# Optimization experiments

Hardware: AMD Instinct MI355X
Metric: run time of the kernel (lower is better)

The kernel has to match this reference:

```python
import jax, jax.numpy as jnp
import numpy as np

N_NODES = 50000
N_EDGES = 800000
IN_C = 64
HID = 128
OUT_C = 2
N_GRAPHS = 64


def setup_inputs() -> dict:
    key = jax.random.key(0)
    ks = jax.random.split(key, 12)
    x = jax.random.normal(ks[0], (N_NODES, IN_C), dtype=jnp.float32)
    edge_index = jax.random.randint(ks[1], (2, N_EDGES), 0, N_NODES, dtype=jnp.int64)
    batch = jnp.sort(jax.random.randint(ks[2], (N_NODES,), 0, N_GRAPHS, dtype=jnp.int64))
    def glorot(k, shape):
        lim = float(np.sqrt(6.0 / (shape[0] + shape[1])))
        return jax.random.uniform(k, shape, dtype=jnp.float32, minval=-lim, maxval=lim)
    return {
        "x": x,
        "edge_index": edge_index,
        "batch": batch,
        "W1": glorot(ks[3], (IN_C, HID)),  "b1": jnp.zeros((HID,), jnp.float32),
        "W2": glorot(ks[4], (HID, HID)),   "b2": jnp.zeros((HID,), jnp.float32),
        "Wm1": glorot(ks[5], (HID, HID)),  "bm1": jnp.zeros((HID,), jnp.float32),
        "Wm2": glorot(ks[6], (HID, OUT_C)), "bm2": jnp.zeros((OUT_C,), jnp.float32),
    }


def reference(x, edge_index, batch, W1, b1, W2, b2, Wm1, bm1, Wm2, bm2):
    N = x.shape[0]
    # GCN normalization with self-loops (PyG GCNConv defaults)
    loops = jnp.arange(N, dtype=edge_index.dtype)
    src = jnp.concatenate([edge_index[0], loops])  # message sources
    dst = jnp.concatenate([edge_index[1], loops])  # aggregation targets
    deg = jax.ops.segment_sum(jnp.ones(dst.shape, x.dtype), dst, num_segments=N)
    dinv = jnp.where(deg > 0, jax.lax.rsqrt(deg), 0.0)
    norm = dinv[src] * dinv[dst]  # [E+N]

    def gcn_conv(h, W, b):
        h = h @ W                         # transform first (PyG order)
        msg = h[src] * norm[:, None]      # gather + normalize
        return jax.ops.segment_sum(msg, dst, num_segments=N) + b  # scatter-add

    h = jax.nn.relu(gcn_conv(x, W1, b1))
    # dropout is identity in eval mode
    h = gcn_conv(h, W2, b2)

    # global mean pool over graphs
    sums = jax.ops.segment_sum(h, batch, num_segments=N_GRAPHS)
    cnt = jax.ops.segment_sum(jnp.ones((N,), h.dtype), batch, num_segments=N_GRAPHS)
    g = sums / jnp.maximum(cnt, 1.0)[:, None]  # [G, HID]

    g = jax.nn.relu(g @ Wm1 + bm1)
    return g @ Wm2 + bm2  # [G, OUT_C]
```

## Files before the change

### kernel.cpp

```cpp
#include <hip/hip_runtime.h>
#include <stdint.h>

#define N_NODES 50000
#define N_EDGES 800000
#define IN_C 64
#define HID 128
#define OUT_C 2
#define N_GRAPHS 64
#define NBUCK 196
#define BCAP 6144
#define ECH 4096

typedef long long i64;
typedef __attribute__((ext_vector_type(8))) short bf8;
typedef __attribute__((ext_vector_type(4))) float f32x4;

__device__ __forceinline__ float bf2f(ushort h) {
    return __uint_as_float(((uint)h) << 16);
}
__device__ __forceinline__ ushort f2bf(float f) {
    uint x = __float_as_uint(f);
    uint r = x + 0x7fffu + ((x >> 16) & 1u);
    return (ushort)(r >> 16);
}
__device__ __forceinline__ float loadf(const void* p, size_t i, int bf) {
    return bf ? bf2f(((const ushort*)p)[i]) : ((const float*)p)[i];
}
__device__ __forceinline__ int clampi(int v, int lo, int hi) {
    return min(max(v, lo), hi);
}

__device__ __forceinline__ int edge_src(const void* ei, int e, int wide) {
    return wide ? (int)((const i64*)ei)[e] : ((const int*)ei)[e];
}
__device__ __forceinline__ int edge_dst(const void* ei, int e, int wide) {
    return wide ? (int)((const i64*)ei)[N_EDGES + e] : ((const int*)ei)[N_EDGES + e];
}
__device__ __forceinline__ i64 batch_at(const void* b, int i, int wide) {
    return wide ? ((const i64*)b)[i] : (i64)((const int*)b)[i];
}

__device__ __forceinline__ void bacc4(float* a, uint2 u) {
    a[0] += bf2f((ushort)(u.x & 0xffffu)); a[1] += bf2f((ushort)(u.x >> 16));
    a[2] += bf2f((ushort)(u.y & 0xffffu)); a[3] += bf2f((ushort)(u.y >> 16));
}
__device__ __forceinline__ uint pk2(float lo, float hi) {
    return ((uint)f2bf(hi) << 16) | (uint)f2bf(lo);
}

__global__ __launch_bounds__(256) void k_init(const uint* __restrict__ braw,
                                              const uint* __restrict__ xraw,
                                              int* __restrict__ bcnt,
                                              float* __restrict__ gbuf,
                                              int* __restrict__ iflag,
                                              int* __restrict__ fflag) {
    int i = blockIdx.x * blockDim.x + threadIdx.x;
    if (i < N_GRAPHS * HID) gbuf[i] = 0.f;
    if (i < NBUCK) bcnt[i] = 0;
    if (blockIdx.x == 0) {
        __shared__ uint si[128];
        __shared__ int sf[256];
        int t = threadIdx.x;
        if (t < 128) si[t] = (t < 100) ? braw[25001 + 2 * t] : 0u;
        uint e = (xraw[t] >> 7) & 0xFFu;
        sf[t] = (e >= 100u && e <= 140u) ? 1 : 0;
        __syncthreads();
        for (int off = 128; off > 0; off >>= 1) {
            if (t < off) {
                sf[t] += sf[t + off];
                if (off <= 64 && t < 64) si[t] |= si[t + off];
            }
            __syncthreads();
        }
        if (t == 0) {
            *iflag = (si[0] == 0u) ? 1 : 0;
            *fflag = (sf[0] >= 192) ? 1 : 0;
        }
    }
}

__global__ __launch_bounds__(1024) void k_binA(const void* __restrict__ ei,
                                               const int* __restrict__ iflag,
                                               const int* __restrict__ fflag,
                                               const void* __restrict__ W1,
                                               const void* __restrict__ W2,
                                               ushort* __restrict__ Wt1,
                                               ushort* __restrict__ Wt2,
                                               int* __restrict__ bcnt,
                                               uint2* __restrict__ bmem) {
    int t = threadIdx.x;
    if (t < 256 && blockIdx.x < (IN_C * HID + HID * HID) / 256) {
        int ff = *fflag;
        int idx = blockIdx.x * 256 + t;
        if (idx < IN_C * HID) {
            int k = idx >> 7, n = idx & 127;
            Wt1[n * IN_C + k] = f2bf(loadf(W1, idx, ff));
        } else {
            int j = idx - IN_C * HID;
            int k = j >> 7, n = j & 127;
            Wt2[n * HID + k] = f2bf(loadf(W2, j, ff));
        }
    }
    int wide = *iflag;
    __shared__ int cnt[NBUCK];
    __shared__ int obase[NBUCK];
    __shared__ int run[NBUCK];
    __shared__ int gbase[NBUCK];
    __shared__ int sc[256];
    __shared__ uint2 stage[ECH];
    int e0 = blockIdx.x * ECH;
    int m = min(ECH, N_EDGES - e0);
    for (int i = t; i < NBUCK; i += 1024) cnt[i] = 0;
    __syncthreads();
    for (int i = t; i < m; i += 1024) {
        int d = edge_dst(ei, e0 + i, wide);
        atomicAdd(&cnt[d >> 8], 1);
    }
    __syncthreads();
    int cv = (t < NBUCK) ? cnt[t] : 0;
    if (t < 256) sc[t] = cv;
    __syncthreads();
    for (int off = 1; off < 256; off <<= 1) {
        int v = (t >= off && t < 256) ? sc[t - off] : 0;
        __syncthreads();
        if (t < 256) sc[t] += v;
        __syncthreads();
    }
    if (t < NBUCK) {
        int ex = sc[t] - cv;
        obase[t] = ex;
        run[t] = ex;
        gbase[t] = (cv > 0) ? atomicAdd(&bcnt[t], cv) : 0;
    }
    __syncthreads();
    for (int i = t; i < m; i += 1024) {
        int s = edge_src(ei, e0 + i, wide);
        int d = edge_dst(ei, e0 + i, wide);
        int slot = atomicAdd(&run[d >> 8], 1);
        uint2 pr; pr.x = (uint)s; pr.y = (uint)d;
        stage[slot] = pr;
    }
    __syncthreads();
    for (int i = t; i < m; i += 1024) {
        uint2 pr = stage[i];
        int b = (int)(pr.y >> 8);
        int pos = gbase[b] + (i - obase[b]);
        if (pos < BCAP) bmem[(size_t)b * BCAP + pos] = pr;
    }
}

__global__ __launch_bounds__(1024) void k_binB(const uint2* __restrict__ bmem,
                                               const int* __restrict__ bcnt,
                                               const void* __restrict__ x,
                                               const int* __restrict__ fflag,
                                               int* __restrict__ offs,
                                               int* __restrict__ csr,
                                               float* __restrict__ dinv,
                                               ushort* __restrict__ Y1) {
    int b = blockIdx.x;
    int t = threadIdx.x;
    int node0 = b << 8;
    __shared__ int sc[256];
    __shared__ int degl[256];
    __shared__ int run[256];
    __shared__ float sdinv[256];
    __shared__ int sbase, scnt;
    __shared__ int stage[BCAP];
    int v = (t < NBUCK) ? bcnt[t] : 0;
    if (t < 256) sc[t] = v;
    __syncthreads();
    for (int off = 1; off < 256; off <<= 1) {
        int u = (t >= off && t < 256) ? sc[t - off] : 0;
        __syncthreads();
        if (t < 256) sc[t] += u;
        __syncthreads();
    }
    if (t == b) {
        int c = clampi(v, 0, BCAP);
        scnt = c;
        sbase = clampi(sc[t] - v, 0, N_EDGES - c);
    }
    if (t < 256) degl[t] = 0;
    __syncthreads();
    int cnt = scnt;
    int base = sbase;
    for (int i = t; i < cnt; i += 1024) {
        uint2 pr = bmem[(size_t)b * BCAP + i];
        atomicAdd(&degl[pr.y & 255], 1);
    }
    __syncthreads();
    int dv = (t < 256) ? degl[t] : 0;
    if (t < 256) sc[t] = dv;
    __syncthreads();
    for (int off = 1; off < 256; off <<= 1) {
        int u = (t >= off && t < 256) ? sc[t - off] : 0;
        __syncthreads();
        if (t < 256) sc[t] += u;
        __syncthreads();
    }
    if (t < 256) {
        int ex = sc[t] - dv;
        run[t] = ex;
        float di = rsqrtf((float)(dv + 1));
        sdinv[t] = di;
        int n = node0 + t;
        if (n < N_NODES) { offs[n] = base + ex; dinv[n] = di; }
    }
    if (b == 0 && t == 0) offs[N_NODES] = N_EDGES;
    __syncthreads();
    for (int i = t; i < cnt; i += 1024) {
        uint2 pr = bmem[(size_t)b * BCAP + i];
        int slot = atomicAdd(&run[pr.y & 255], 1);
        stage[clampi(slot, 0, BCAP - 1)] = (int)pr.x;
    }
    __syncthreads();
    for (int i = t; i < cnt; i += 1024) csr[base + i] = stage[i];
    int ff = *fflag;
    for (int idx = t; idx < 256 * (IN_C / 4); idx += 1024) {
        int nl = idx >> 4, c4 = (idx & 15) * 4;
        int nn = node0 + nl;
        if (nn < N_NODES) {
            float x0, x1, x2, x3;
            if (ff) {
                ushort4 u = *(const ushort4*)((const ushort*)x + (size_t)nn * IN_C + c4);
                x0 = bf2f(u.x); x1 = bf2f(u.y); x2 = bf2f(u.z); x3 = bf2f(u.w);
            } else {
                float4 vv = *(const float4*)((const float*)x + (size_t)nn * IN_C + c4);
                x0 = vv.x; x1 = vv.y; x2 = vv.z; x3 = vv.w;
            }
            float di = sdinv[nl];
            ushort4 o;
            o.x = f2bf(x0 * di); o.y = f2bf(x1 * di);
            o.z = f2bf(x2 * di); o.w = f2bf(x3 * di);
            int g = c4 >> 5;
            *(ushort4*)(Y1 + ((size_t)g * N_NODES + nn) * 32 + (c4 & 31)) = o;
        }
    }
}

template <int SHIFT>
__global__ __launch_bounds__(256) void k_aggS(const ushort* __restrict__ src,
                                              const float* __restrict__ dinv,
                                              const int* __restrict__ offs,
                                              const int* __restrict__ csr,
                                              ushort* __restrict__ out) {
    int g = blockIdx.x & ((1 << SHIFT) - 1);
    int chunk = blockIdx.x >> SHIFT;
    int n = (chunk * 256 + (int)threadIdx.x) >> 3;
    int lane = threadIdx.x & 7;
    if (n >= N_NODES) return;
    const uint2* s2 = (const uint2*)(src + (size_t)g * N_NODES * 32);
    size_t rb = (size_t)n * 8 + lane;
    float a[4];
    {
        uint2 su = s2[rb];
        a[0] = bf2f((ushort)(su.x & 0xffffu)); a[1] = bf2f((ushort)(su.x >> 16));
        a[2] = bf2f((ushort)(su.y & 0xffffu)); a[3] = bf2f((ushort)(su.y >> 16));
    }
    int s = offs[n];
    int e = min(offs[n + 1], s + 4096);
    int i = s;
    for (; i + 8 <= e; i += 8) {
        uint2 u[8];
#pragma unroll
        for (int k = 0; k < 8; k++)
            u[k] = s2[(size_t)csr[i + k] * 8 + lane];
#pragma unroll
        for (int k = 0; k < 8; k++) bacc4(a, u[k]);
    }
    for (; i < e; i++) bacc4(a, s2[(size_t)csr[i] * 8 + lane]);
    float dv = dinv[n];
    uint2 o;
    o.x = pk2(a[0] * dv, a[1] * dv);
    o.y = pk2(a[2] * dv, a[3] * dv);
    ((uint2*)(out + (size_t)g * N_NODES * 32))[rb] = o;
}

template <int K>
__global__ __launch_bounds__(256) void k_gemm_f(const ushort* __restrict__ A,
                                                const ushort* __restrict__ Wt,
                                                const int* __restrict__ fflag,
                                                const float* __restrict__ dinv,
                                                const void* __restrict__ bias,
                                                ushort* __restrict__ out) {
    int ff = *fflag;
    int wave = threadIdx.x >> 6;
    int lane = threadIdx.x & 63;
    int m16 = lane & 15;
    int q = lane >> 4;
    int rowbase = blockIdx.x * 64 + wave * 16;
    int arow = min(rowbase + m16, N_NODES - 1);

    f32x4 acc[8];
#pragma unroll
    for (int t = 0; t < 8; t++) acc[t] = (f32x4){0.f, 0.f, 0.f, 0.f};
#pragma unroll
    for (int kc = 0; kc < K; kc += 32) {
        bf8 a = *(const bf8*)(A + ((size_t)(kc >> 5) * N_NODES + arow) * 32 + q * 8);
#pragma unroll
        for (int t = 0; t < 8; t++) {
            bf8 b = *(const bf8*)(Wt + (size_t)(t * 16 + m16) * K + kc + q * 8);
            acc[t] = __builtin_amdgcn_mfma_f32_16x16x32_bf16(a, b, acc[t], 0, 0, 0);
        }
    }
    float dv[4];
    int rowok[4];
#pragma unroll
    for (int r = 0; r < 4; r++) {
        int row = rowbase + q * 4 + r;
        rowok[r] = (row < N_NODES);
        dv[r] = rowok[r] ? dinv[row] : 1.f;
    }
#pragma unroll
    for (int t = 0; t < 8; t++) {
        int col = t * 16 + m16;
        float bv = loadf(bias, col, ff);
        ushort* og = out + (size_t)(col >> 5) * N_NODES * 32 + (col & 31);
#pragma unroll
        for (int r = 0; r < 4; r++) {
            int row = rowbase + q * 4 + r;
            if (rowok[r]) {
                float v = fmaxf(acc[t][r] + bv, 0.f) * dv[r];
                og[(size_t)row * 32] = f2bf(v);
            }
        }
    }
}

__global__ __launch_bounds__(256) void k_gemm_pool(const ushort* __restrict__ A,
                                                   const ushort* __restrict__ Wt,
                                                   const void* __restrict__ batch,
                                                   const int* __restrict__ iflag,
                                                   float* __restrict__ gsum) {
    const int K = HID;
    int wide = *iflag;
    int tid = threadIdx.x;
    int wave = tid >> 6;
    int lane = tid & 63;
    int m16 = lane & 15;
    int q = lane >> 4;
    int rowbase = blockIdx.x * 64 + wave * 16;
    int arow = min(rowbase + m16, N_NODES - 1);

    __shared__ float sacc[64][HID];
    __shared__ int sbg[64];

    if (tid < 64) {
        int n = blockIdx.x * 64 + tid;
        int g = (n < N_NODES) ? (int)batch_at(batch, n, wide) : -1;
        sbg[tid] = (g < 0 || g >= N_GRAPHS) ? -1 : g;
    }
    f32x4 acc[8];
#pragma unroll
    for (int t = 0; t < 8; t++) acc[t] = (f32x4){0.f, 0.f, 0.f, 0.f};
#pragma unroll
    for (int kc = 0; kc < K; kc += 32) {
        bf8 a = *(const bf8*)(A + ((size_t)(kc >> 5) * N_NODES + arow) * 32 + q * 8);
#pragma unroll
        for (int t = 0; t < 8; t++) {
            bf8 b = *(const bf8*)(Wt + (size_t)(t * 16 + m16) * K + kc + q * 8);
            acc[t] = __builtin_amdgcn_mfma_f32_16x16x32_bf16(a, b, acc[t], 0, 0, 0);
        }
    }
#pragma unroll
    for (int t = 0; t < 8; t++) {
        int col = t * 16 + m16;
#pragma unroll
        for (int r = 0; r < 4; r++) {
            int rl = wave * 16 + q * 4 + r;
            int row = rowbase + q * 4 + r;
            sacc[rl][col] = (row < N_NODES) ? acc[t][r] : 0.f;
        }
    }
    __syncthreads();
    int col = tid & 127;
    int half = tid >> 7;
    int gcur = -1;
    float a = 0.f;
    for (int r = half * 32; r < half * 32 + 32; r++) {
        int g = sbg[r];
        if (g != gcur) {
            if (gcur >= 0) atomicAdd(&gsum[gcur * HID + col], a);
            a = 0.f;
            gcur = g;
        }
        a += sacc[r][col];
    }
    if (gcur >= 0) atomicAdd(&gsum[gcur * HID + col], a);
}

__global__ void k_mlp(const float* __restrict__ gsum, const void* __restrict__ batch,
                      const int* __restrict__ iflag, const void* __restrict__ b2,
                      const void* __restrict__ Wm1, const void* __restrict__ bm1,
                      const void* __restrict__ Wm2, const void* __restrict__ bm2,
                      const int* __restrict__ fflag, float* __restrict__ out) {
    int ff = *fflag;
    int wide = *iflag;
    int gr = blockIdx.x;
    int c = threadIdx.x;
    int lo = 0, hi = N_NODES;
    while (lo < hi) { int m = (lo + hi) >> 1; if (batch_at(batch, m, wide) < (i64)gr) lo = m + 1; else hi = m; }
    int s = lo;
    lo = s; hi = N_NODES;
    while (lo < hi) { int m = (lo + hi) >> 1; if (batch_at(batch, m, wide) < (i64)(gr + 1)) lo = m + 1; else hi = m; }
    float cnt = (float)(lo - s);

    __shared__ float sg[HID];
    __shared__ float r0[HID], r1[HID];
    sg[c] = gsum[gr * HID + c] / fmaxf(cnt, 1.0f) + loadf(b2, c, ff);
    __syncthreads();
    float acc = loadf(bm1, c, ff);
#pragma unroll 8
    for (int k = 0; k < HID; k++) acc += sg[k] * loadf(Wm1, k * HID + c, ff);
    float hid = fmaxf(acc, 0.f);
    r0[c] = hid * loadf(Wm2, c * OUT_C + 0, ff);
    r1[c] = hid * loadf(Wm2, c * OUT_C + 1, ff);
    __syncthreads();
    for (int off = 64; off > 0; off >>= 1) {
        if (c < off) { r0[c] += r0[c + off]; r1[c] += r1[c + off]; }
        __syncthreads();
    }
    if (c == 0) {
        out[gr * OUT_C + 0] = r0[0] + loadf(bm2, 0, ff);
        out[gr * OUT_C + 1] = r1[0] + loadf(bm2, 1, ff);
    }
}


extern "C" void kernel_launch(void* const* d_in, const int* in_sizes, int n_in,
                              void* d_out, int out_size, void* d_ws, size_t ws_size,
                              hipStream_t stream) {
    const void* x     = d_in[0];
    const void* ei    = d_in[1];
    const void* batch = d_in[2];
    const void* W1  = d_in[3];
    const void* b1  = d_in[4];
    const void* W2  = d_in[5];
    const void* b2  = d_in[6];
    const void* Wm1 = d_in[7];
    const void* bm1 = d_in[8];
    const void* Wm2 = d_in[9];
    const void* bm2 = d_in[10];

    char* p = (char*)d_ws;
    auto alloc = [&](size_t bytes) {
        char* r = p;
        p += (bytes + 255) & ~(size_t)255;
        return r;
    };
    int*    iflag  = (int*)alloc(4);
    int*    fflag  = (int*)alloc(4);
    int*    bcnt   = (int*)alloc(NBUCK * 4);
    uint2*  bmem   = (uint2*)alloc((size_t)NBUCK * BCAP * 8);
    float*  dinv   = (float*)alloc(N_NODES * 4);
    int*    offs   = (int*)alloc((N_NODES + 1) * 4);
    int*    csr    = (int*)alloc(N_EDGES * 4);
    ushort* Wt1    = (ushort*)alloc(IN_C * HID * 2);
    ushort* Wt2    = (ushort*)alloc(HID * HID * 2);
    ushort* Y1g    = (ushort*)alloc((size_t)N_NODES * IN_C * 2);
    ushort* Mg     = (ushort*)alloc((size_t)N_NODES * IN_C * 2);
    ushort* h1g    = (ushort*)alloc((size_t)N_NODES * HID * 2);
    ushort* N2g    = (ushort*)alloc((size_t)N_NODES * HID * 2);
    float*  gbuf   = (float*)alloc(N_GRAPHS * HID * 4);

    k_init<<<(N_GRAPHS * HID + 255) / 256, 256, 0, stream>>>(
        (const uint*)batch, (const uint*)x, bcnt, gbuf, iflag, fflag);
    k_binA<<<(N_EDGES + ECH - 1) / ECH, 1024, 0, stream>>>(
        ei, iflag, fflag, W1, W2, Wt1, Wt2, bcnt, bmem);
    k_binB<<<NBUCK, 1024, 0, stream>>>(bmem, bcnt, x, fflag, offs, csr, dinv, Y1g);

    int cpg = (N_NODES * 8 + 255) / 256;
    k_aggS<1><<<cpg * 2, 256, 0, stream>>>(Y1g, dinv, offs, csr, Mg);
    k_gemm_f<IN_C><<<(N_NODES + 63) / 64, 256, 0, stream>>>(Mg, Wt1, fflag, dinv, b1, h1g);
    k_aggS<2><<<cpg * 4, 256, 0, stream>>>(h1g, dinv, offs, csr, N2g);
    k_gemm_pool<<<(N_NODES + 63) / 64, 256, 0, stream>>>(N2g, Wt2, batch, iflag, gbuf);

    k_mlp<<<N_GRAPHS, HID, 0, stream>>>(gbuf, batch, iflag, b2, Wm1, bm1, Wm2, bm2, fflag, (float*)d_out);
}
```

Baseline: 204.4 us.

## Replace two-pass bucket binning CSR build with global-atomic degree/scan/fill

Swaps the bucketed two-kernel CSR construction (local-histogram binning into per-bucket staging, then per-bucket sort) for a classic three-step build: global atomic degree count, single-block prefix scan, and atomic-cursor fill. This removes the large bmem staging buffer and its extra round trip through memory. In exchange it adds heavy global atomic contention on 50k counters and a serial single-block scan. It also makes the CSR neighbour order within each row nondeterministic, which changes memory locality in the later aggregation passes.

```diff
diff --git a/kernel.cpp b/kernel.cpp
--- a/kernel.cpp
+++ b/kernel.cpp
@@ -7,9 +7,7 @@
 #define HID 128
 #define OUT_C 2
 #define N_GRAPHS 64
-#define NBUCK 196
-#define BCAP 6144
-#define ECH 4096
+#define SCH 49
 
 typedef long long i64;
 typedef __attribute__((ext_vector_type(8))) short bf8;
@@ -50,13 +48,14 @@
 
 __global__ __launch_bounds__(256) void k_init(const uint* __restrict__ braw,
                                               const uint* __restrict__ xraw,
-                                              int* __restrict__ bcnt,
+                                              int* __restrict__ deg,
                                               float* __restrict__ gbuf,
                                               int* __restrict__ iflag,
                                               int* __restrict__ fflag) {
     int i = blockIdx.x * blockDim.x + threadIdx.x;
+    int stride = gridDim.x * blockDim.x;
+    for (int j = i; j < N_NODES; j += stride) deg[j] = 0;
     if (i < N_GRAPHS * HID) gbuf[i] = 0.f;
-    if (i < NBUCK) bcnt[i] = 0;
     if (blockIdx.x == 0) {
         __shared__ uint si[128];
         __shared__ int sf[256];
@@ -79,17 +78,16 @@
     }
 }
 
-__global__ __launch_bounds__(1024) void k_binA(const void* __restrict__ ei,
-                                               const int* __restrict__ iflag,
-                                               const int* __restrict__ fflag,
-                                               const void* __restrict__ W1,
-                                               const void* __restrict__ W2,
-                                               ushort* __restrict__ Wt1,
-                                               ushort* __restrict__ Wt2,
-                                               int* __restrict__ bcnt,
-                                               uint2* __restrict__ bmem) {
+__global__ __launch_bounds__(256) void k_deg(const void* __restrict__ ei,
+                                             const int* __restrict__ iflag,
+                                             const int* __restrict__ fflag,
+                                             const void* __restrict__ W1,
+                                             const void* __restrict__ W2,
+                                             ushort* __restrict__ Wt1,
+                                             ushort* __restrict__ Wt2,
+                                             int* __restrict__ deg) {
     int t = threadIdx.x;
-    if (t < 256 && blockIdx.x < (IN_C * HID + HID * HID) / 256) {
+    if (blockIdx.x < (IN_C * HID + HID * HID) / 256) {
         int ff = *fflag;
         int idx = blockIdx.x * 256 + t;
         if (idx < IN_C * HID) {
@@ -102,139 +100,76 @@
         }
     }
     int wide = *iflag;
-    __shared__ int cnt[NBUCK];
-    __shared__ int obase[NBUCK];
-    __shared__ int run[NBUCK];
-    __shared__ int gbase[NBUCK];
-    __shared__ int sc[256];
-    __shared__ uint2 stage[ECH];
-    int e0 = blockIdx.x * ECH;
-    int m = min(ECH, N_EDGES - e0);
-    for (int i = t; i < NBUCK; i += 1024) cnt[i] = 0;
+    int i0 = blockIdx.x * 256 + t;
+    int stride = gridDim.x * 256;
+    for (int e = i0; e < N_EDGES; e += stride) {
+        int d = edge_dst(ei, e, wide);
+        atomicAdd(&deg[clampi(d, 0, N_NODES - 1)], 1);
+    }
+}
+
+__global__ __launch_bounds__(1024) void k_scan(const int* __restrict__ deg,
+                                               int* __restrict__ offs,
+                                               int* __restrict__ cursor,
+                                               float* __restrict__ dinv) {
+    __shared__ int sc[1024];
+    int t = threadIdx.x;
+    int lo = t * SCH, hi = min(lo + SCH, N_NODES);
+    int s = 0;
+    for (int i = lo; i < hi; i++) s += deg[i];
+    sc[t] = s;
     __syncthreads();
-    for (int i = t; i < m; i += 1024) {
-        int d = edge_dst(ei, e0 + i, wide);
-        atomicAdd(&cnt[d >> 8], 1);
-    }
-    __syncthreads();
-    int cv = (t < NBUCK) ? cnt[t] : 0;
-    if (t < 256) sc[t] = cv;
-    __syncthreads();
-    for (int off = 1; off < 256; off <<= 1) {
-        int v = (t >= off && t < 256) ? sc[t - off] : 0;
+    for (int off = 1; off < 1024; off <<= 1) {
+        int v = (t >= off) ? sc[t - off] : 0;
         __syncthreads();
-        if (t < 256) sc[t] += v;
+        sc[t] += v;
         __syncthreads();
     }
-    if (t < NBUCK) {
-        int ex = sc[t] - cv;
-        obase[t] = ex;
-        run[t] = ex;
-        gbase[t] = (cv > 0) ? atomicAdd(&bcnt[t], cv) : 0;
-    }
-    __syncthreads();
-    for (int i = t; i < m; i += 1024) {
-        int s = edge_src(ei, e0 + i, wide);
-        int d = edge_dst(ei, e0 + i, wide);
-        int slot = atomicAdd(&run[d >> 8], 1);
-        uint2 pr; pr.x = (uint)s; pr.y = (uint)d;
-        stage[slot] = pr;
-    }
-    __syncthreads();
-    for (int i = t; i < m; i += 1024) {
-        uint2 pr = stage[i];
-        int b = (int)(pr.y >> 8);
-        int pos = gbase[b] + (i - obase[b]);
-        if (pos < BCAP) bmem[(size_t)b * BCAP + pos] = pr;
-    }
-}
-
-__global__ __launch_bounds__(1024) void k_binB(const uint2* __restrict__ bmem,
-                                               const int* __restrict__ bcnt,
-                                               const void* __restrict__ x,
-                                               const int* __restrict__ fflag,
-                                               int* __restrict__ offs,
-                                               int* __restrict__ csr,
-                                               float* __restrict__ dinv,
-                                               ushort* __restrict__ Y1) {
-    int b = blockIdx.x;
-    int t = threadIdx.x;
-    int node0 = b << 8;
-    __shared__ int sc[256];
-    __shared__ int degl[256];
-    __shared__ int run[256];
-    __shared__ float sdinv[256];
-    __shared__ int sbase, scnt;
-    __shared__ int stage[BCAP];
-    int v = (t < NBUCK) ? bcnt[t] : 0;
-    if (t < 256) sc[t] = v;
-    __syncthreads();
-    for (int off = 1; off < 256; off <<= 1) {
-        int u = (t >= off && t < 256) ? sc[t - off] : 0;
-        __syncthreads();
-        if (t < 256) sc[t] += u;
-        __syncthreads();
-    }
-    if (t == b) {
-        int c = clampi(v, 0, BCAP);
-        scnt = c;
-        sbase = clampi(sc[t] - v, 0, N_EDGES - c);
-    }
-    if (t < 256) degl[t] = 0;
-    __syncthreads();
-    int cnt = scnt;
-    int base = sbase;
-    for (int i = t; i < cnt; i += 1024) {
-        uint2 pr = bmem[(size_t)b * BCAP + i];
-        atomicAdd(&degl[pr.y & 255], 1);
-    }
-    __syncthreads();
-    int dv = (t < 256) ? degl[t] : 0;
-    if (t < 256) sc[t] = dv;
-    __syncthreads();
-    for (int off = 1; off < 256; off <<= 1) {
-        int u = (t >= off && t < 256) ? sc[t - off] : 0;
-        __syncthreads();
-        if (t < 256) sc[t] += u;
-        __syncthreads();
-    }
-    if (t < 256) {
-        int ex = sc[t] - dv;
-        run[t] = ex;
-        float di = rsqrtf((float)(dv + 1));
-        sdinv[t] = di;
-        int n = node0 + t;
-        if (n < N_NODES) { offs[n] = base + ex; dinv[n] = di; }
-    }
-    if (b == 0 && t == 0) offs[N_NODES] = N_EDGES;
-    __syncthreads();
-    for (int i = t; i < cnt; i += 1024) {
-        uint2 pr = bmem[(size_t)b * BCAP + i];
-        int slot = atomicAdd(&run[pr.y & 255], 1);
-        stage[clampi(slot, 0, BCAP - 1)] = (int)pr.x;
-    }
-    __syncthreads();
-    for (int i = t; i < cnt; i += 1024) csr[base + i] = stage[i];
+    int run = (t > 0) ? sc[t - 1] : 0;
+    for (int i = lo; i < hi; i++) {
+        int d = deg[i];
+        offs[i] = run;
+        cursor[i] = run;
+        dinv[i] = rsqrtf((float)(d + 1));
+        run += d;
+    }
+    if (t == 0) offs[N_NODES] = N_EDGES;
+}
+
+__global__ __launch_bounds__(256) void k_fill(const void* __restrict__ ei,
+                                              const int* __restrict__ iflag,
+                                              const int* __restrict__ fflag,
+                                              const void* __restrict__ x,
+                                              const float* __restrict__ dinv,
+                                              int* __restrict__ cursor,
+                                              int* __restrict__ csr,
+                                              ushort* __restrict__ Y1) {
+    int wide = *iflag;
+    int t0 = blockIdx.x * 256 + (int)threadIdx.x;
+    int stride = gridDim.x * 256;
+    for (int e = t0; e < N_EDGES; e += stride) {
+        int sN = edge_src(ei, e, wide);
+        int d = edge_dst(ei, e, wide);
+        int pos = atomicAdd(&cursor[clampi(d, 0, N_NODES - 1)], 1);
+        csr[clampi(pos, 0, N_EDGES - 1)] = clampi(sN, 0, N_NODES - 1);
+    }
     int ff = *fflag;
-    for (int idx = t; idx < 256 * (IN_C / 4); idx += 1024) {
-        int nl = idx >> 4, c4 = (idx & 15) * 4;
-        int nn = node0 + nl;
-        if (nn < N_NODES) {
-            float x0, x1, x2, x3;
-            if (ff) {
-                ushort4 u = *(const ushort4*)((const ushort*)x + (size_t)nn * IN_C + c4);
-                x0 = bf2f(u.x); x1 = bf2f(u.y); x2 = bf2f(u.z); x3 = bf2f(u.w);
-            } else {
-                float4 vv = *(const float4*)((const float*)x + (size_t)nn * IN_C + c4);
-                x0 = vv.x; x1 = vv.y; x2 = vv.z; x3 = vv.w;
-            }
-            float di = sdinv[nl];
-            ushort4 o;
-            o.x = f2bf(x0 * di); o.y = f2bf(x1 * di);
-            o.z = f2bf(x2 * di); o.w = f2bf(x3 * di);
-            int g = c4 >> 5;
-            *(ushort4*)(Y1 + ((size_t)g * N_NODES + nn) * 32 + (c4 & 31)) = o;
-        }
+    for (int idx = t0; idx < N_NODES * (IN_C / 4); idx += stride) {
+        int nn = idx >> 4, c4 = (idx & 15) * 4;
+        float x0, x1, x2, x3;
+        if (ff) {
+            ushort4 u = *(const ushort4*)((const ushort*)x + (size_t)nn * IN_C + c4);
+            x0 = bf2f(u.x); x1 = bf2f(u.y); x2 = bf2f(u.z); x3 = bf2f(u.w);
+        } else {
+            float4 vv = *(const float4*)((const float*)x + (size_t)nn * IN_C + c4);
+            x0 = vv.x; x1 = vv.y; x2 = vv.z; x3 = vv.w;
+        }
+        float di = dinv[nn];
+        ushort4 o;
+        o.x = f2bf(x0 * di); o.y = f2bf(x1 * di);
+        o.z = f2bf(x2 * di); o.w = f2bf(x3 * di);
+        int g = c4 >> 5;
+        *(ushort4*)(Y1 + ((size_t)g * N_NODES + nn) * 32 + (c4 & 31)) = o;
     }
 }
 
@@ -450,8 +385,8 @@
     };
     int*    iflag  = (int*)alloc(4);
     int*    fflag  = (int*)alloc(4);
-    int*    bcnt   = (int*)alloc(NBUCK * 4);
-    uint2*  bmem   = (uint2*)alloc((size_t)NBUCK * BCAP * 8);
+    int*    deg    = (int*)alloc(N_NODES * 4);
+    int*    cursor = (int*)alloc(N_NODES * 4);
     float*  dinv   = (float*)alloc(N_NODES * 4);
     int*    offs   = (int*)alloc((N_NODES + 1) * 4);
     int*    csr    = (int*)alloc(N_EDGES * 4);
@@ -463,11 +398,11 @@
     ushort* N2g    = (ushort*)alloc((size_t)N_NODES * HID * 2);
     float*  gbuf   = (float*)alloc(N_GRAPHS * HID * 4);
 
-    k_init<<<(N_GRAPHS * HID + 255) / 256, 256, 0, stream>>>(
-        (const uint*)batch, (const uint*)x, bcnt, gbuf, iflag, fflag);
-    k_binA<<<(N_EDGES + ECH - 1) / ECH, 1024, 0, stream>>>(
-        ei, iflag, fflag, W1, W2, Wt1, Wt2, bcnt, bmem);
-    k_binB<<<NBUCK, 1024, 0, stream>>>(bmem, bcnt, x, fflag, offs, csr, dinv, Y1g);
+    k_init<<<256, 256, 0, stream>>>(
+        (const uint*)batch, (const uint*)x, deg, gbuf, iflag, fflag);
+    k_deg<<<1024, 256, 0, stream>>>(ei, iflag, fflag, W1, W2, Wt1, Wt2, deg);
+    k_scan<<<1, 1024, 0, stream>>>(deg, offs, cursor, dinv);
+    k_fill<<<1024, 256, 0, stream>>>(ei, iflag, fflag, x, dinv, cursor, csr, Y1g);
 
     int cpg = (N_NODES * 8 + 255) / 256;
     k_aggS<1><<<cpg * 2, 256, 0, stream>>>(Y1g, dinv, offs, csr, Mg);
```

After: 413.1 us. +102.1%, slower.

## Pack edge bins and CSR into narrower types and drop init kernel

Applied to the files above, without the earlier changes.

Packs each binned edge into one 32-bit word (16-bit source, local dst, bucket id) and stores CSR column indices as 16-bit values, roughly halving the traffic for binning and the gathers that follow. The init kernel is replaced by memsets, and each kernel re-derives the dtype flags with a per-block warp-shuffle probe, so no flag has to be stored in and reloaded from global memory. Bias b1 is pre-converted to fp32. A 16-bit source index cannot hold N_NODES=50000 above 65535, and it fits here only because the node count is below that.

```diff
diff --git a/kernel.cpp b/kernel.cpp
--- a/kernel.cpp
+++ b/kernel.cpp
@@ -29,7 +29,6 @@
 __device__ __forceinline__ int clampi(int v, int lo, int hi) {
     return min(max(v, lo), hi);
 }
-
 __device__ __forceinline__ int edge_src(const void* ei, int e, int wide) {
     return wide ? (int)((const i64*)ei)[e] : ((const int*)ei)[e];
 }
@@ -39,7 +38,6 @@
 __device__ __forceinline__ i64 batch_at(const void* b, int i, int wide) {
     return wide ? ((const i64*)b)[i] : (i64)((const int*)b)[i];
 }
-
 __device__ __forceinline__ void bacc4(float* a, uint2 u) {
     a[0] += bf2f((ushort)(u.x & 0xffffu)); a[1] += bf2f((ushort)(u.x >> 16));
     a[2] += bf2f((ushort)(u.y & 0xffffu)); a[3] += bf2f((ushort)(u.y >> 16));
@@ -48,49 +46,51 @@
     return ((uint)f2bf(hi) << 16) | (uint)f2bf(lo);
 }
 
-__global__ __launch_bounds__(256) void k_init(const uint* __restrict__ braw,
-                                              const uint* __restrict__ xraw,
-                                              int* __restrict__ bcnt,
-                                              float* __restrict__ gbuf,
-                                              int* __restrict__ iflag,
-                                              int* __restrict__ fflag) {
-    int i = blockIdx.x * blockDim.x + threadIdx.x;
-    if (i < N_GRAPHS * HID) gbuf[i] = 0.f;
-    if (i < NBUCK) bcnt[i] = 0;
-    if (blockIdx.x == 0) {
-        __shared__ uint si[128];
-        __shared__ int sf[256];
-        int t = threadIdx.x;
-        if (t < 128) si[t] = (t < 100) ? braw[25001 + 2 * t] : 0u;
-        uint e = (xraw[t] >> 7) & 0xFFu;
-        sf[t] = (e >= 100u && e <= 140u) ? 1 : 0;
-        __syncthreads();
-        for (int off = 128; off > 0; off >>= 1) {
-            if (t < off) {
-                sf[t] += sf[t + off];
-                if (off <= 64 && t < 64) si[t] |= si[t + off];
-            }
-            __syncthreads();
-        }
-        if (t == 0) {
-            *iflag = (si[0] == 0u) ? 1 : 0;
-            *fflag = (sf[0] >= 192) ? 1 : 0;
-        }
-    }
+__device__ __forceinline__ void block_probe(const uint* __restrict__ braw,
+                                            const uint* __restrict__ xraw,
+                                            int& wide, int& ff) {
+    __shared__ int s_if, s_ff;
+    if (threadIdx.x < 64) {
+        int l = threadIdx.x;
+        uint io = 0u;
+        int fc = 0;
+#pragma unroll
+        for (int j = 0; j < 4; j++) {
+            int t = l + 64 * j;
+            if (t < 100) io |= braw[25001 + 2 * t];
+            uint e = (xraw[t] >> 7) & 0xFFu;
+            fc += (e >= 100u && e <= 140u) ? 1 : 0;
+        }
+#pragma unroll
+        for (int off = 32; off > 0; off >>= 1) {
+            io |= (uint)__shfl_down((int)io, off);
+            fc += __shfl_down(fc, off);
+        }
+        if (l == 0) {
+            s_if = (io == 0u) ? 1 : 0;
+            s_ff = (fc >= 192) ? 1 : 0;
+        }
+    }
+    __syncthreads();
+    wide = s_if;
+    ff = s_ff;
 }
 
 __global__ __launch_bounds__(1024) void k_binA(const void* __restrict__ ei,
-                                               const int* __restrict__ iflag,
-                                               const int* __restrict__ fflag,
+                                               const uint* __restrict__ braw,
+                                               const uint* __restrict__ xraw,
                                                const void* __restrict__ W1,
                                                const void* __restrict__ W2,
+                                               const void* __restrict__ b1,
                                                ushort* __restrict__ Wt1,
                                                ushort* __restrict__ Wt2,
+                                               float* __restrict__ b1f,
                                                int* __restrict__ bcnt,
-                                               uint2* __restrict__ bmem) {
+                                               uint* __restrict__ bmem) {
+    int wide, ff;
+    block_probe(braw, xraw, wide, ff);
     int t = threadIdx.x;
     if (t < 256 && blockIdx.x < (IN_C * HID + HID * HID) / 256) {
-        int ff = *fflag;
         int idx = blockIdx.x * 256 + t;
         if (idx < IN_C * HID) {
             int k = idx >> 7, n = idx & 127;
@@ -101,13 +101,14 @@
             Wt2[n * HID + k] = f2bf(loadf(W2, j, ff));
         }
     }
-    int wide = *iflag;
+    if (blockIdx.x == 96 && t < HID) b1f[t] = loadf(b1, t, ff);
+
     __shared__ int cnt[NBUCK];
     __shared__ int obase[NBUCK];
     __shared__ int run[NBUCK];
     __shared__ int gbase[NBUCK];
     __shared__ int sc[256];
-    __shared__ uint2 stage[ECH];
+    __shared__ uint stage[ECH];
     int e0 = blockIdx.x * ECH;
     int m = min(ECH, N_EDGES - e0);
     for (int i = t; i < NBUCK; i += 1024) cnt[i] = 0;
@@ -137,26 +138,29 @@
         int s = edge_src(ei, e0 + i, wide);
         int d = edge_dst(ei, e0 + i, wide);
         int slot = atomicAdd(&run[d >> 8], 1);
-        uint2 pr; pr.x = (uint)s; pr.y = (uint)d;
-        stage[slot] = pr;
+        uint pr = (uint)clampi(s, 0, N_NODES - 1) |
+                  ((uint)(d & 255) << 16) | ((uint)(d >> 8) << 24);
+        stage[clampi(slot, 0, ECH - 1)] = pr;
     }
     __syncthreads();
     for (int i = t; i < m; i += 1024) {
-        uint2 pr = stage[i];
-        int b = (int)(pr.y >> 8);
+        uint pr = stage[i];
+        int b = (int)(pr >> 24);
         int pos = gbase[b] + (i - obase[b]);
         if (pos < BCAP) bmem[(size_t)b * BCAP + pos] = pr;
     }
 }
 
-__global__ __launch_bounds__(1024) void k_binB(const uint2* __restrict__ bmem,
+__global__ __launch_bounds__(1024) void k_binB(const uint* __restrict__ bmem,
                                                const int* __restrict__ bcnt,
                                                const void* __restrict__ x,
-                                               const int* __restrict__ fflag,
+                                               const uint* __restrict__ braw,
                                                int* __restrict__ offs,
-                                               int* __restrict__ csr,
+                                               ushort* __restrict__ csr,
                                                float* __restrict__ dinv,
                                                ushort* __restrict__ Y1) {
+    int wide, ff;
+    block_probe(braw, (const uint*)x, wide, ff);
     int b = blockIdx.x;
     int t = threadIdx.x;
     int node0 = b << 8;
@@ -165,7 +169,7 @@
     __shared__ int run[256];
     __shared__ float sdinv[256];
     __shared__ int sbase, scnt;
-    __shared__ int stage[BCAP];
+    __shared__ ushort stage[BCAP];
     int v = (t < NBUCK) ? bcnt[t] : 0;
     if (t < 256) sc[t] = v;
     __syncthreads();
@@ -185,8 +189,8 @@
     int cnt = scnt;
     int base = sbase;
     for (int i = t; i < cnt; i += 1024) {
-        uint2 pr = bmem[(size_t)b * BCAP + i];
-        atomicAdd(&degl[pr.y & 255], 1);
+        uint pr = bmem[(size_t)b * BCAP + i];
+        atomicAdd(&degl[(pr >> 16) & 255], 1);
     }
     __syncthreads();
     int dv = (t < 256) ? degl[t] : 0;
@@ -209,13 +213,12 @@
     if (b == 0 && t == 0) offs[N_NODES] = N_EDGES;
     __syncthreads();
     for (int i = t; i < cnt; i += 1024) {
-        uint2 pr = bmem[(size_t)b * BCAP + i];
-        int slot = atomicAdd(&run[pr.y & 255], 1);
-        stage[clampi(slot, 0, BCAP - 1)] = (int)pr.x;
+        uint pr = bmem[(size_t)b * BCAP + i];
+        int slot = atomicAdd(&run[(pr >> 16) & 255], 1);
+        stage[clampi(slot, 0, BCAP - 1)] = (ushort)(pr & 0xFFFFu);
     }
     __syncthreads();
     for (int i = t; i < cnt; i += 1024) csr[base + i] = stage[i];
-    int ff = *fflag;
     for (int idx = t; idx < 256 * (IN_C / 4); idx += 1024) {
         int nl = idx >> 4, c4 = (idx & 15) * 4;
         int nn = node0 + nl;
@@ -242,7 +245,7 @@
 __global__ __launch_bounds__(256) void k_aggS(const ushort* __restrict__ src,
                                               const float* __restrict__ dinv,
                                               const int* __restrict__ offs,
-                                              const int* __restrict__ csr,
+                                              const ushort* __restrict__ csr,
                                               ushort* __restrict__ out) {
     int g = blockIdx.x & ((1 << SHIFT) - 1);
     int chunk = blockIdx.x >> SHIFT;
@@ -279,11 +282,9 @@
 template <int K>
 __global__ __launch_bounds__(256) void k_gemm_f(const ushort* __restrict__ A,
                                                 const ushort* __restrict__ Wt,
-                                                const int* __restrict__ fflag,
                                                 const float* __restrict__ dinv,
-                                                const void* __restrict__ bias,
+                                                const float* __restrict__ b1f,
                                                 ushort* __restrict__ out) {
-    int ff = *fflag;
     int wave = threadIdx.x >> 6;
     int lane = threadIdx.x & 63;
     int m16 = lane & 15;
@@ -314,7 +315,7 @@
 #pragma unroll
     for (int t = 0; t < 8; t++) {
         int col = t * 16 + m16;
-        float bv = loadf(bias, col, ff);
+        float bv = b1f[col];
         ushort* og = out + (size_t)(col >> 5) * N_NODES * 32 + (col & 31);
 #pragma unroll
         for (int r = 0; r < 4; r++) {
@@ -330,10 +331,11 @@
 __global__ __launch_bounds__(256) void k_gemm_pool(const ushort* __restrict__ A,
                                                    const ushort* __restrict__ Wt,
                                                    const void* __restrict__ batch,
-                                                   const int* __restrict__ iflag,
+                                                   const uint* __restrict__ xraw,
                                                    float* __restrict__ gsum) {
+    int wide, ff;
+    block_probe((const uint*)batch, xraw, wide, ff);
     const int K = HID;
-    int wide = *iflag;
     int tid = threadIdx.x;
     int wave = tid >> 6;
     int lane = tid & 63;
@@ -389,13 +391,14 @@
     if (gcur >= 0) atomicAdd(&gsum[gcur * HID + col], a);
 }
 
-__global__ void k_mlp(const float* __restrict__ gsum, const void* __restrict__ batch,
-                      const int* __restrict__ iflag, const void* __restrict__ b2,
+__global__ __launch_bounds__(128) void k_mlp(const float* __restrict__ gsum,
+                      const void* __restrict__ batch, const uint* __restrict__ xraw,
+                      const void* __restrict__ b2,
                       const void* __restrict__ Wm1, const void* __restrict__ bm1,
                       const void* __restrict__ Wm2, const void* __restrict__ bm2,
-                      const int* __restrict__ fflag, float* __restrict__ out) {
-    int ff = *fflag;
-    int wide = *iflag;
+                      float* __restrict__ out) {
+    int wide, ff;
+    block_probe((const uint*)batch, xraw, wide, ff);
     int gr = blockIdx.x;
     int c = threadIdx.x;
     int lo = 0, hi = N_NODES;
@@ -448,32 +451,33 @@
         p += (bytes + 255) & ~(size_t)255;
         return r;
     };
-    int*    iflag  = (int*)alloc(4);
-    int*    fflag  = (int*)alloc(4);
     int*    bcnt   = (int*)alloc(NBUCK * 4);
-    uint2*  bmem   = (uint2*)alloc((size_t)NBUCK * BCAP * 8);
+    uint*   bmem   = (uint*)alloc((size_t)NBUCK * BCAP * 4);
     float*  dinv   = (float*)alloc(N_NODES * 4);
     int*    offs   = (int*)alloc((N_NODES + 1) * 4);
-    int*    csr    = (int*)alloc(N_EDGES * 4);
+    ushort* csr    = (ushort*)alloc(N_EDGES * 2);
     ushort* Wt1    = (ushort*)alloc(IN_C * HID * 2);
     ushort* Wt2    = (ushort*)alloc(HID * HID * 2);
+    float*  b1f    = (float*)alloc(HID * 4);
     ushort* Y1g    = (ushort*)alloc((size_t)N_NODES * IN_C * 2);
     ushort* Mg     = (ushort*)alloc((size_t)N_NODES * IN_C * 2);
     ushort* h1g    = (ushort*)alloc((size_t)N_NODES * HID * 2);
     ushort* N2g    = (ushort*)alloc((size_t)N_NODES * HID * 2);
     float*  gbuf   = (float*)alloc(N_GRAPHS * HID * 4);
 
-    k_init<<<(N_GRAPHS * HID + 255) / 256, 256, 0, stream>>>(
-        (const uint*)batch, (const uint*)x, bcnt, gbuf, iflag, fflag);
+    hipMemsetAsync(bcnt, 0, NBUCK * 4, stream);
+    hipMemsetAsync(gbuf, 0, N_GRAPHS * HID * 4, stream);
+
     k_binA<<<(N_EDGES + ECH - 1) / ECH, 1024, 0, stream>>>(
-        ei, iflag, fflag, W1, W2, Wt1, Wt2, bcnt, bmem);
-    k_binB<<<NBUCK, 1024, 0, stream>>>(bmem, bcnt, x, fflag, offs, csr, dinv, Y1g);
+        ei, (const uint*)batch, (const uint*)x, W1, W2, b1, Wt1, Wt2, b1f, bcnt, bmem);
+    k_binB<<<NBUCK, 1024, 0, stream>>>(bmem, bcnt, x, (const uint*)batch,
+                                       offs, csr, dinv, Y1g);
 
     int cpg = (N_NODES * 8 + 255) / 256;
     k_aggS<1><<<cpg * 2, 256, 0, stream>>>(Y1g, dinv, offs, csr, Mg);
-    k_gemm_f<IN_C><<<(N_NODES + 63) / 64, 256, 0, stream>>>(Mg, Wt1, fflag, dinv, b1, h1g);
+    k_gemm_f<IN_C><<<(N_NODES + 63) / 64, 256, 0, stream>>>(Mg, Wt1, dinv, b1f, h1g);
     k_aggS<2><<<cpg * 4, 256, 0, stream>>>(h1g, dinv, offs, csr, N2g);
-    k_gemm_pool<<<(N_NODES + 63) / 64, 256, 0, stream>>>(N2g, Wt2, batch, iflag, gbuf);
-
-    k_mlp<<<N_GRAPHS, HID, 0, stream>>>(gbuf, batch, iflag, b2, Wm1, bm1, Wm2, bm2, fflag, (float*)d_out);
-}
+    k_gemm_pool<<<(N_NODES + 63) / 64, 256, 0, stream>>>(N2g, Wt2, batch, (const uint*)x, gbuf);
+
+    k_mlp<<<N_GRAPHS, 128, 0, stream>>>(gbuf, batch, (const uint*)x, b2, Wm1, bm1, Wm2, bm2, (float*)d_out);
+}
```

Measured after the change: 205.9 us. About the same (+0.7%).
